# Kernel tuning notes

Hardware: AMD Instinct MI355X
Metric: run time of the kernel (lower is better)

## Reference

```python
import jax, jax.numpy as jnp
import numpy as np

HID = 256
NPOS = 1000
NEG = -1e9  # finite stand-in for -inf in masked softmax


def _sinusoid_table(n_pos, d):
    pos = np.arange(n_pos, dtype=np.float64)[:, None]
    j = np.arange(d)[None, :]
    angle = pos / np.power(10000.0, 2 * (j // 2) / d)
    table = np.where(j % 2 == 0, np.sin(angle), np.cos(angle))
    return jnp.asarray(table, dtype=jnp.float32)  # [n_pos, d]


def setup_inputs() -> dict:
    key = jax.random.key(0)
    k1, k2 = jax.random.split(key)
    B, Tx, Ty = 32, 512, 1000
    return {
        "x_h": jax.random.normal(k1, (B, HID, Tx), dtype=jnp.float32),
        "y_h": jax.random.normal(k2, (B, HID, Ty), dtype=jnp.float32),
        "x_mask": jnp.ones((B, Tx), dtype=bool),
        "y_mask": jnp.ones((B, Ty), dtype=bool),
        "sigma": jnp.float32(0.2),
    }


def reference(x_h, y_h, x_mask, y_mask, sigma):
    B, hid, Tx = x_h.shape
    Ty = y_h.shape[-1]
    dt = x_h.dtype
    pos = _sinusoid_table(NPOS, HID)
    x_h = x_h + pos[:Tx].T[None]  # [B, hid, Tx]
    y_h = y_h + pos[:Ty].T[None]  # [B, hid, Ty]
    xm = x_mask.astype(dt)
    ym = y_mask.astype(dt)

    # ---- compute_PI ----
    scores = jnp.einsum('bht,bhs->bts', y_h, x_h) / np.sqrt(float(hid))  # [B,Ty,Tx]
    scores = jnp.where(x_mask[:, None, :], scores, NEG)
    alpha = jax.nn.softmax(scores, axis=-1)
    p = jnp.arange(Tx, dtype=dt)[None] * xm  # [B,Tx]
    pi_dummy = jnp.einsum('bts,bs->bt', alpha, p)  # [B,Ty]
    delta = jnp.maximum(pi_dummy[:, 1:] - pi_dummy[:, :-1], 0.0)
    delta = jnp.concatenate([jnp.zeros((B, 1), dt), delta], axis=-1) * ym
    pi_f = jnp.cumsum(delta, axis=-1) * ym
    pi_b = -jnp.flip(jnp.cumsum(jnp.flip(delta, -1), axis=-1), -1)
    pi = pi_f + pi_b
    last_pi = jnp.clip(jnp.max(pi, axis=-1), 1e-8, None)[:, None]
    first_pi = pi[:, 0:1]
    max_pi = jnp.sum(xm, axis=-1)[:, None] - 1.0
    pi = (pi - first_pi) / (last_pi - first_pi) * max_pi  # [B,Ty]

    # ---- e and boundaries ----
    q = jnp.arange(Ty, dtype=dt)[None] * ym  # [B,Ty]

    def align(centers):  # centers [B,Tx] -> [B,Tx]
        en = -((pi[:, None, :] - centers[:, :, None]) ** 2) * sigma  # [B,Tx,Ty]
        en = jnp.where(y_mask[:, None, :], en, NEG)
        beta = jax.nn.softmax(en, axis=2)
        return jnp.einsum('bty,by->bt', beta, q) * xm

    e = align(p)
    boundary_idx = jnp.maximum(p - 0.5, 0.0)
    a = align(boundary_idx)
    a_real = jnp.concatenate([jnp.zeros((B, 1), dt), a[:, 1:]], axis=-1)
    max_x = jnp.sum(x_mask.astype(jnp.int32), axis=-1) - 1
    max_y = jnp.sum(y_mask.astype(jnp.int32), axis=-1) - 1
    b = jnp.concatenate([a_real[:, 1:], jnp.zeros((B, 1), dt)], axis=-1)
    b_real = b.at[jnp.arange(B), max_x].set(max_y.astype(dt))
    return (e, a_real, b_real)
```

## Files before the change

### kernel.cpp

```cpp
#include <hip/hip_runtime.h>


typedef unsigned short ushortT;
typedef __attribute__((ext_vector_type(8))) __bf16 bf16x8;
typedef __attribute__((ext_vector_type(4))) float f32x4;

#define XB_OFF 0
#define YB_OFF 8388608
#define PID_OFF 25165824

#define GLDS(gp, lp)                                                        \
  __builtin_amdgcn_global_load_lds(                                         \
      (const __attribute__((address_space(1))) unsigned int*)(gp),          \
      (__attribute__((address_space(3))) unsigned int*)(lp), 16, 0, 0)

__device__ inline ushortT f2bf(float f) {
  unsigned int u = __float_as_uint(f);
  u += 0x7fffu + ((u >> 16) & 1u);
  return (ushortT)(u >> 16);
}

__device__ inline float4 ntload4(const float* p) {
  const float4* q = reinterpret_cast<const float4*>(p);
  float4 v;
  v.x = __builtin_nontemporal_load(&q->x);
  v.y = __builtin_nontemporal_load(&q->y);
  v.z = __builtin_nontemporal_load(&q->z);
  v.w = __builtin_nontemporal_load(&q->w);
  return v;
}

__global__ __launch_bounds__(256) void k_prep(const float* __restrict__ xh,
                                              const float* __restrict__ yh,
                                              ushortT* __restrict__ Xb,
                                              ushortT* __restrict__ Yb) {
  __shared__ float tile[64][65];
  const int tid = threadIdx.x;
  const float C = 0.07195578415606394f;
  if (blockIdx.x < 1024) {
    const int id = blockIdx.x;
    const int b = id & 31, rem = id >> 5, ht = rem >> 3, st = rem & 7;
#pragma unroll
    for (int r = 0; r < 4; ++r) {
      const int hr = r * 16 + (tid >> 4);
      const int h = ht * 64 + hr;
      const int sc = st * 64 + (tid & 15) * 4;
      float4 v = ntload4(xh + ((size_t)(b * 256 + h)) * 512 + sc);
      const float freq = __expf(-C * (float)(h >> 1));
      float p[4];
#pragma unroll
      for (int i = 0; i < 4; ++i) {
        float ang = (float)(sc + i) * freq;
        p[i] = (h & 1) ? __cosf(ang) : __sinf(ang);
      }
      tile[hr][(tid & 15) * 4 + 0] = v.x + p[0];
      tile[hr][(tid & 15) * 4 + 1] = v.y + p[1];
      tile[hr][(tid & 15) * 4 + 2] = v.z + p[2];
      tile[hr][(tid & 15) * 4 + 3] = v.w + p[3];
    }
    __syncthreads();
#pragma unroll
    for (int r = 0; r < 4; ++r) {
      const int srow = r * 16 + (tid >> 4);
      const int h4 = (tid & 15) * 4;
      ushort4 q;
      q.x = f2bf(tile[h4 + 0][srow]);
      q.y = f2bf(tile[h4 + 1][srow]);
      q.z = f2bf(tile[h4 + 2][srow]);
      q.w = f2bf(tile[h4 + 3][srow]);
      *reinterpret_cast<ushort4*>(
          Xb + ((size_t)(b * 512 + st * 64 + srow)) * 256 + ht * 64 + h4) = q;
    }
  } else {
    const int id = blockIdx.x - 1024;
    const int b = id & 31, rem = id >> 5, ht = rem >> 4, tt = rem & 15;
#pragma unroll
    for (int r = 0; r < 4; ++r) {
      const int hr = r * 16 + (tid >> 4);
      const int h = ht * 64 + hr;
      const int tc = tt * 64 + (tid & 15) * 4;
      float4 v = make_float4(0.f, 0.f, 0.f, 0.f);
      if (tc < 1000)
        v = ntload4(yh + ((size_t)(b * 256 + h)) * 1000 + tc);
      const float freq = __expf(-C * (float)(h >> 1));
      float p[4];
#pragma unroll
      for (int i = 0; i < 4; ++i) {
        float ang = (float)(tc + i) * freq;
        p[i] = (h & 1) ? __cosf(ang) : __sinf(ang);
      }
      tile[hr][(tid & 15) * 4 + 0] = v.x + p[0];
      tile[hr][(tid & 15) * 4 + 1] = v.y + p[1];
      tile[hr][(tid & 15) * 4 + 2] = v.z + p[2];
      tile[hr][(tid & 15) * 4 + 3] = v.w + p[3];
    }
    __syncthreads();
#pragma unroll
    for (int r = 0; r < 4; ++r) {
      const int trow = r * 16 + (tid >> 4);
      const int t = tt * 64 + trow;
      if (t < 1000) {
        const int h4 = (tid & 15) * 4;
        ushort4 q;
        q.x = f2bf(tile[h4 + 0][trow]);
        q.y = f2bf(tile[h4 + 1][trow]);
        q.z = f2bf(tile[h4 + 2][trow]);
        q.w = f2bf(tile[h4 + 3][trow]);
        *reinterpret_cast<ushort4*>(
            Yb + ((size_t)(b * 1024 + t)) * 256 + ht * 64 + h4) = q;
      }
    }
  }
}

__global__ __launch_bounds__(512, 2) void k_scores5(const ushortT* __restrict__ Xb,
                                                    const ushortT* __restrict__ Yb,
                                                    float* __restrict__ pid) {
  __shared__ __align__(16) unsigned char sm[40960];
  const int tid = threadIdx.x;
  const int w = tid >> 6, l = tid & 63;
  const int wr = w >> 2, wc = w & 3;
  const int quad = l >> 4, lo = l & 15;
  const int b = blockIdx.x & 31, tt = blockIdx.x >> 5, t0 = tt * 128;

  f32x4 acc[4][8];
#pragma unroll
  for (int rb = 0; rb < 4; ++rb)
#pragma unroll
    for (int cb = 0; cb < 8; ++cb) acc[rb][cb] = (f32x4){0.f, 0.f, 0.f, 0.f};

  const int arow = tid >> 2, ach = tid & 3;
  const ushortT* gA = Yb + ((size_t)(b * 1024 + t0 + arow)) * 256 + ach * 8;
  const ushortT* gB = Xb + ((size_t)(b * 512 + arow)) * 256 + ach * 8;

  for (int kc = 0; kc < 8; ++kc) {
    const int k0 = kc * 32;
    GLDS(gA + k0, sm + tid * 16);
#pragma unroll
    for (int j = 0; j < 4; ++j)
      GLDS(gB + (size_t)(j * 128) * 256 + k0, sm + 8192 + j * 8192 + tid * 16);
    __syncthreads();
    bf16x8 af[4], bfr[8];
#pragma unroll
    for (int rb = 0; rb < 4; ++rb)
      af[rb] = *reinterpret_cast<const bf16x8*>(
          sm + (wr * 64 + rb * 16 + lo) * 64 + quad * 16);
#pragma unroll
    for (int cb = 0; cb < 8; ++cb)
      bfr[cb] = *reinterpret_cast<const bf16x8*>(
          sm + 8192 + (wc * 128 + cb * 16 + lo) * 64 + quad * 16);
#pragma unroll
    for (int cb = 0; cb < 8; ++cb)
#pragma unroll
      for (int rb = 0; rb < 4; ++rb)
        acc[rb][cb] = __builtin_amdgcn_mfma_f32_16x16x32_bf16(
            af[rb], bfr[cb], acc[rb][cb], 0, 0, 0);
    __syncthreads();
  }

  float* red = (float*)sm;
#pragma unroll
  for (int rb = 0; rb < 4; ++rb) {
#pragma unroll
    for (int i = 0; i < 4; ++i) {
      const int row = wr * 64 + rb * 16 + quad * 4 + i;
      float m = acc[rb][0][i];
#pragma unroll
      for (int cb = 1; cb < 8; ++cb) m = fmaxf(m, acc[rb][cb][i]);
#pragma unroll
      for (int msk = 1; msk < 16; msk <<= 1)
        m = fmaxf(m, __shfl_xor(m, msk, 64));
      if (lo == 0) red[wc * 128 + row] = m;
    }
  }
  __syncthreads();
#pragma unroll
  for (int rb = 0; rb < 4; ++rb) {
#pragma unroll
    for (int i = 0; i < 4; ++i) {
      const int row = wr * 64 + rb * 16 + quad * 4 + i;
      const float rm = fmaxf(fmaxf(red[row], red[128 + row]),
                             fmaxf(red[256 + row], red[384 + row]));
      float s = 0.f, sy = 0.f;
#pragma unroll
      for (int cb = 0; cb < 8; ++cb) {
        float e = __expf((acc[rb][cb][i] - rm) * 0.0625f);
        s += e;
        sy = fmaf(e, (float)(wc * 128 + cb * 16 + lo), sy);
      }
#pragma unroll
      for (int msk = 1; msk < 16; msk <<= 1) {
        s += __shfl_xor(s, msk, 64);
        sy += __shfl_xor(sy, msk, 64);
      }
      if (lo == 0) {
        red[512 + wc * 128 + row] = s;
        red[1024 + wc * 128 + row] = sy;
      }
    }
  }
  __syncthreads();
  if (tid < 128) {
    const int t = t0 + tid;
    if (t < 1000) {
      float s = red[512 + tid] + red[640 + tid] + red[768 + tid] +
                red[896 + tid];
      float sy = red[1024 + tid] + red[1152 + tid] + red[1280 + tid] +
                 red[1408 + tid];
      pid[b * 1000 + t] = sy / s;
    }
  }
}

__global__ __launch_bounds__(512) void k_scanalign(const float* __restrict__ pid,
                                                   const float* __restrict__ sigma,
                                                   float* __restrict__ out) {
  __shared__ float carr[1000];
  __shared__ float pin_s[1000];
  __shared__ float wtot[8];
  const int tid = threadIdx.x, wv = tid >> 6, l = tid & 63;
  const int b = blockIdx.x & 31, t0 = (blockIdx.x >> 5) * 64;

  float d[2] = {0.f, 0.f}, c[2];
#pragma unroll
  for (int k = 0; k < 2; ++k) {
    int t = tid * 2 + k;
    if (t > 0 && t < 1000)
      d[k] = fmaxf(pid[b * 1000 + t] - pid[b * 1000 + t - 1], 0.f);
  }
  c[0] = d[0];
  c[1] = c[0] + d[1];
  float x = c[1];
#pragma unroll
  for (int off = 1; off < 64; off <<= 1) {
    float n = __shfl_up(x, off, 64);
    if (l >= off) x += n;
  }
  if (l == 63) wtot[wv] = x;
  __syncthreads();
  float woff = 0.f;
#pragma unroll
  for (int ww = 0; ww < 8; ++ww)
    if (ww < wv) woff += wtot[ww];
  float excl = woff + x - c[1];
  c[0] += excl;
  c[1] += excl;
#pragma unroll
  for (int k = 0; k < 2; ++k) {
    int t = tid * 2 + k;
    if (t < 1000) carr[t] = c[k];
  }
  __syncthreads();
  const float scale = 511.0f / (fmaxf(carr[998], 1e-8f) + carr[999]);
#pragma unroll
  for (int k = 0; k < 2; ++k) {
    int t = tid * 2 + k;
    if (t < 1000) pin_s[t] = (carr[t] + (t ? carr[t - 1] : 0.f)) * scale;
  }
  __syncthreads();

  const float sg = sigma[0];
  const float dmax = __fsqrt_rn(88.0f / sg);
  for (int i = 0; i < 8; ++i) {
    const int t = t0 + wv * 8 + i;
    const float ce = (float)t;
    const float ca = fmaxf(ce - 0.5f, 0.f);
    const float lov = ca - dmax, hiv = ce + dmax;
    int lo = 0, cnt = 1000;
    while (cnt > 0) {
      int st = cnt >> 1;
      if (pin_s[lo + st] < lov) { lo += st + 1; cnt -= st + 1; }
      else cnt = st;
    }
    int hi = lo, cnt2 = 1000 - lo;
    while (cnt2 > 0) {
      int st = cnt2 >> 1;
      if (pin_s[hi + st] <= hiv) { hi += st + 1; cnt2 -= st + 1; }
      else cnt2 = st;
    }
    float s1 = 0.f, sy1 = 0.f, s2 = 0.f, sy2 = 0.f;
    for (int y = lo + l; y < hi; y += 64) {
      float pv = pin_s[y];
      float d1 = pv - ce, d2 = pv - ca;
      float w1 = __expf(-sg * d1 * d1);
      float w2 = __expf(-sg * d2 * d2);
      s1 += w1; sy1 = fmaf(w1, (float)y, sy1);
      s2 += w2; sy2 = fmaf(w2, (float)y, sy2);
    }
#pragma unroll
    for (int m = 1; m < 64; m <<= 1) {
      s1 += __shfl_xor(s1, m, 64);
      sy1 += __shfl_xor(sy1, m, 64);
      s2 += __shfl_xor(s2, m, 64);
      sy2 += __shfl_xor(sy2, m, 64);
    }
    if (l == 0) {
      float e = sy1 / s1;
      float a = sy2 / s2;
      out[b * 512 + t] = e;
      out[16384 + b * 512 + t] = (t == 0) ? 0.f : a;
      if (t >= 1) out[32768 + b * 512 + (t - 1)] = a;
      if (t == 511) out[32768 + b * 512 + 511] = 999.0f;
    }
  }
}

extern "C" void kernel_launch(void* const* d_in, const int* in_sizes, int n_in,
                              void* d_out, int out_size, void* d_ws, size_t ws_size,
                              hipStream_t stream) {
  (void)in_sizes; (void)n_in; (void)out_size; (void)ws_size;
  const float* xh = (const float*)d_in[0];
  const float* yh = (const float*)d_in[1];
  const float* sigma = (const float*)d_in[4];
  ushortT* Xb = (ushortT*)((char*)d_ws + XB_OFF);
  ushortT* Yb = (ushortT*)((char*)d_ws + YB_OFF);
  float* pid = (float*)((char*)d_ws + PID_OFF);
  float* out = (float*)d_out;

  k_prep<<<3072, 256, 0, stream>>>(xh, yh, Xb, Yb);
  k_scores5<<<256, 512, 0, stream>>>(Xb, Yb, pid);
  k_scanalign<<<256, 512, 0, stream>>>(pid, sigma, out);
}
```

Before: 137.6 us.

## Fuse scan and alignment into scores kernel via last-block election per batch

Removes the separate scan/align kernel by having the last finishing scores block of each batch, detected with an atomic counter, perform the cumulative scan and both alignments for all 512 rows. This eliminates a kernel launch and the redundant per-block rescans of pid. In exchange, alignment for each batch runs on one block serially, which reduces parallelism and may lengthen the tail. It also adds a memset to reset the counters.

```diff
diff --git a/kernel.cpp b/kernel.cpp
--- a/kernel.cpp
+++ b/kernel.cpp
@@ -8,6 +8,7 @@
 #define XB_OFF 0
 #define YB_OFF 8388608
 #define PID_OFF 25165824
+#define CTR_OFF 25296896
 
 #define GLDS(gp, lp)                                                        \
   __builtin_amdgcn_global_load_lds(                                         \
@@ -113,10 +114,12 @@
   }
 }
 
-__global__ __launch_bounds__(512, 2) void k_scores5(const ushortT* __restrict__ Xb,
-                                                    const ushortT* __restrict__ Yb,
-                                                    float* __restrict__ pid) {
+__global__ __launch_bounds__(512, 2) void k_scores6(
+    const ushortT* __restrict__ Xb, const ushortT* __restrict__ Yb,
+    const float* __restrict__ sigma, float* __restrict__ pid,
+    unsigned* __restrict__ done, float* __restrict__ out) {
   __shared__ __align__(16) unsigned char sm[40960];
+  __shared__ int elect;
   const int tid = threadIdx.x;
   const int w = tid >> 6, l = tid & 63;
   const int wr = w >> 2, wc = w & 3;
@@ -210,97 +213,107 @@
       pid[b * 1000 + t] = sy / s;
     }
   }
-}
-
-__global__ __launch_bounds__(512) void k_scanalign(const float* __restrict__ pid,
-                                                   const float* __restrict__ sigma,
-                                                   float* __restrict__ out) {
-  __shared__ float carr[1000];
-  __shared__ float pin_s[1000];
-  __shared__ float wtot[8];
-  const int tid = threadIdx.x, wv = tid >> 6, l = tid & 63;
-  const int b = blockIdx.x & 31, t0 = (blockIdx.x >> 5) * 64;
-
-  float d[2] = {0.f, 0.f}, c[2];
-#pragma unroll
-  for (int k = 0; k < 2; ++k) {
-    int t = tid * 2 + k;
-    if (t > 0 && t < 1000)
-      d[k] = fmaxf(pid[b * 1000 + t] - pid[b * 1000 + t - 1], 0.f);
-  }
-  c[0] = d[0];
-  c[1] = c[0] + d[1];
-  float x = c[1];
-#pragma unroll
-  for (int off = 1; off < 64; off <<= 1) {
-    float n = __shfl_up(x, off, 64);
-    if (l >= off) x += n;
-  }
-  if (l == 63) wtot[wv] = x;
+
   __syncthreads();
-  float woff = 0.f;
-#pragma unroll
-  for (int ww = 0; ww < 8; ++ww)
-    if (ww < wv) woff += wtot[ww];
-  float excl = woff + x - c[1];
-  c[0] += excl;
-  c[1] += excl;
-#pragma unroll
-  for (int k = 0; k < 2; ++k) {
-    int t = tid * 2 + k;
-    if (t < 1000) carr[t] = c[k];
+  if (tid == 0) {
+    __threadfence();
+    unsigned old = __hip_atomic_fetch_add(&done[b], 1u, __ATOMIC_ACQ_REL,
+                                          __HIP_MEMORY_SCOPE_AGENT);
+    elect = (old == 7u);
+    if (elect) __threadfence();
   }
   __syncthreads();
-  const float scale = 511.0f / (fmaxf(carr[998], 1e-8f) + carr[999]);
-#pragma unroll
-  for (int k = 0; k < 2; ++k) {
-    int t = tid * 2 + k;
-    if (t < 1000) pin_s[t] = (carr[t] + (t ? carr[t - 1] : 0.f)) * scale;
-  }
-  __syncthreads();
-
-  const float sg = sigma[0];
-  const float dmax = __fsqrt_rn(88.0f / sg);
-  for (int i = 0; i < 8; ++i) {
-    const int t = t0 + wv * 8 + i;
-    const float ce = (float)t;
-    const float ca = fmaxf(ce - 0.5f, 0.f);
-    const float lov = ca - dmax, hiv = ce + dmax;
-    int lo = 0, cnt = 1000;
-    while (cnt > 0) {
-      int st = cnt >> 1;
-      if (pin_s[lo + st] < lov) { lo += st + 1; cnt -= st + 1; }
-      else cnt = st;
-    }
-    int hi = lo, cnt2 = 1000 - lo;
-    while (cnt2 > 0) {
-      int st = cnt2 >> 1;
-      if (pin_s[hi + st] <= hiv) { hi += st + 1; cnt2 -= st + 1; }
-      else cnt2 = st;
-    }
-    float s1 = 0.f, sy1 = 0.f, s2 = 0.f, sy2 = 0.f;
-    for (int y = lo + l; y < hi; y += 64) {
-      float pv = pin_s[y];
-      float d1 = pv - ce, d2 = pv - ca;
-      float w1 = __expf(-sg * d1 * d1);
-      float w2 = __expf(-sg * d2 * d2);
-      s1 += w1; sy1 = fmaf(w1, (float)y, sy1);
-      s2 += w2; sy2 = fmaf(w2, (float)y, sy2);
-    }
-#pragma unroll
-    for (int m = 1; m < 64; m <<= 1) {
-      s1 += __shfl_xor(s1, m, 64);
-      sy1 += __shfl_xor(sy1, m, 64);
-      s2 += __shfl_xor(s2, m, 64);
-      sy2 += __shfl_xor(sy2, m, 64);
-    }
-    if (l == 0) {
-      float e = sy1 / s1;
-      float a = sy2 / s2;
-      out[b * 512 + t] = e;
-      out[16384 + b * 512 + t] = (t == 0) ? 0.f : a;
-      if (t >= 1) out[32768 + b * 512 + (t - 1)] = a;
-      if (t == 511) out[32768 + b * 512 + 511] = 999.0f;
+  if (!elect) return;
+
+  {
+    const int wv = w;
+    float* carr = (float*)sm;
+    float* pin_s = (float*)sm + 1024;
+    float* wtot = (float*)sm + 2048;
+
+    float d[2] = {0.f, 0.f}, c[2];
+#pragma unroll
+    for (int k = 0; k < 2; ++k) {
+      int t = tid * 2 + k;
+      if (t > 0 && t < 1000)
+        d[k] = fmaxf(pid[b * 1000 + t] - pid[b * 1000 + t - 1], 0.f);
+    }
+    c[0] = d[0];
+    c[1] = c[0] + d[1];
+    float x = c[1];
+#pragma unroll
+    for (int off = 1; off < 64; off <<= 1) {
+      float n = __shfl_up(x, off, 64);
+      if (l >= off) x += n;
+    }
+    if (l == 63) wtot[wv] = x;
+    __syncthreads();
+    float woff = 0.f;
+#pragma unroll
+    for (int ww = 0; ww < 8; ++ww)
+      if (ww < wv) woff += wtot[ww];
+    float excl = woff + x - c[1];
+    c[0] += excl;
+    c[1] += excl;
+#pragma unroll
+    for (int k = 0; k < 2; ++k) {
+      int t = tid * 2 + k;
+      if (t < 1000) carr[t] = c[k];
+    }
+    __syncthreads();
+    const float scale = 511.0f / (fmaxf(carr[998], 1e-8f) + carr[999]);
+#pragma unroll
+    for (int k = 0; k < 2; ++k) {
+      int t = tid * 2 + k;
+      if (t < 1000) pin_s[t] = (c[k] + (t ? carr[t - 1] : 0.f)) * scale;
+    }
+    __syncthreads();
+
+    const float sg = sigma[0];
+    const float dmax = __fsqrt_rn(88.0f / sg);
+    for (int tc2 = 0; tc2 < 8; ++tc2) {
+      for (int i = 0; i < 8; ++i) {
+        const int t = tc2 * 64 + wv * 8 + i;
+        const float ce = (float)t;
+        const float ca = fmaxf(ce - 0.5f, 0.f);
+        const float lov = ca - dmax, hiv = ce + dmax;
+        int lo2 = 0, cnt = 1000;
+        while (cnt > 0) {
+          int st = cnt >> 1;
+          if (pin_s[lo2 + st] < lov) { lo2 += st + 1; cnt -= st + 1; }
+          else cnt = st;
+        }
+        int hi = lo2, cnt2 = 1000 - lo2;
+        while (cnt2 > 0) {
+          int st = cnt2 >> 1;
+          if (pin_s[hi + st] <= hiv) { hi += st + 1; cnt2 -= st + 1; }
+          else cnt2 = st;
+        }
+        float s1 = 0.f, sy1 = 0.f, s2 = 0.f, sy2 = 0.f;
+        for (int y = lo2 + l; y < hi; y += 64) {
+          float pv = pin_s[y];
+          float d1 = pv - ce, d2 = pv - ca;
+          float w1 = __expf(-sg * d1 * d1);
+          float w2 = __expf(-sg * d2 * d2);
+          s1 += w1; sy1 = fmaf(w1, (float)y, sy1);
+          s2 += w2; sy2 = fmaf(w2, (float)y, sy2);
+        }
+#pragma unroll
+        for (int m = 1; m < 64; m <<= 1) {
+          s1 += __shfl_xor(s1, m, 64);
+          sy1 += __shfl_xor(sy1, m, 64);
+          s2 += __shfl_xor(s2, m, 64);
+          sy2 += __shfl_xor(sy2, m, 64);
+        }
+        if (l == 0) {
+          float e = sy1 / s1;
+          float a = sy2 / s2;
+          out[b * 512 + t] = e;
+          out[16384 + b * 512 + t] = (t == 0) ? 0.f : a;
+          if (t >= 1) out[32768 + b * 512 + (t - 1)] = a;
+          if (t == 511) out[32768 + b * 512 + 511] = 999.0f;
+        }
+      }
     }
   }
 }
@@ -315,9 +328,10 @@
   ushortT* Xb = (ushortT*)((char*)d_ws + XB_OFF);
   ushortT* Yb = (ushortT*)((char*)d_ws + YB_OFF);
   float* pid = (float*)((char*)d_ws + PID_OFF);
+  unsigned* done = (unsigned*)((char*)d_ws + CTR_OFF);
   float* out = (float*)d_out;
 
+  hipMemsetAsync(done, 0, 128, stream);
   k_prep<<<3072, 256, 0, stream>>>(xh, yh, Xb, Yb);
-  k_scores5<<<256, 512, 0, stream>>>(Xb, Yb, pid);
-  k_scanalign<<<256, 512, 0, stream>>>(pid, sigma, out);
-}
+  k_scores6<<<256, 512, 0, stream>>>(Xb, Yb, sigma, pid, done, out);
+}
```

Measured after the change: 245.2 us. 78.3% more time.
